# Optimization experiments

Hardware: AMD Instinct MI355X
Metric: run time of the kernel (lower is better)

## Reference

```python
import jax, jax.numpy as jnp
import numpy as np

HEAD_SIZE = 128
B, L = 4, 4096

def setup_inputs() -> dict:
    key = jax.random.key(0)
    k1, k2, k3 = jax.random.split(key, 3)
    return {
        "key": jax.random.normal(k1, (B, L, HEAD_SIZE), dtype=jnp.float32),
        "query": jax.random.normal(k2, (B, L, HEAD_SIZE), dtype=jnp.float32),
        "value": jax.random.normal(k3, (B, L, HEAD_SIZE), dtype=jnp.float32),
    }

def reference(key, query, value):
    # attention scores: [B, L, L]
    scale = 1.0 / jnp.sqrt(jnp.asarray(HEAD_SIZE, dtype=query.dtype))
    att = jnp.einsum("bqd,bkd->bqk", query, key) * scale
    # causal mask (tril): positions k > q get -inf
    causal = jnp.tril(jnp.ones((att.shape[1], att.shape[2]), dtype=bool))
    att = jnp.where(causal[None, :, :], att, jnp.array(-jnp.inf, dtype=att.dtype))
    logits = jax.nn.softmax(att, axis=-1)
    # dropout omitted (eval mode / deterministic reference)
    out = jnp.einsum("bqk,bkd->bqd", logits, value)
    return out
```

## Files before the change

kernel.cpp:

```cpp
#include <hip/hip_runtime.h>

#define BB 4
#define LL 4096
#define DD 128

typedef __attribute__((ext_vector_type(8))) short short8;
typedef __attribute__((ext_vector_type(4))) float f32x4;

typedef __attribute__((address_space(1))) const unsigned int gas_u32;
typedef __attribute__((address_space(3))) unsigned int las_u32;

__device__ __forceinline__ void gload_lds16(const void* g, void* l) {
  __builtin_amdgcn_global_load_lds((gas_u32*)g, (las_u32*)l, 16, 0, 0);
}

__device__ __forceinline__ unsigned short f2bf(float x) {
  union { float f; unsigned int u; } c; c.f = x;
  unsigned int r = (c.u + 0x7FFFu + ((c.u >> 16) & 1u)) >> 16;
  return (unsigned short)r;
}
__device__ __forceinline__ float bf2f(unsigned short h) {
  union { unsigned int u; float f; } c; c.u = (unsigned int)h << 16;
  return c.f;
}

__host__ __device__ __forceinline__ int slotBase(int p) {
  int g2 = (p - 4) >> 2, w2 = (p - 4) & 3;
  return 2 * g2 * g2 + 6 * g2 + w2 * (g2 + 2);
}

__global__ __launch_bounds__(256) void prep(const float* __restrict__ K,
                                            const float* __restrict__ V,
                                            unsigned short* __restrict__ Kb,
                                            unsigned short* __restrict__ Vt) {
  __shared__ unsigned short tile[64 * 130];
  int b  = blockIdx.x >> 6;
  int kt = (blockIdx.x & 63) << 6;
  int t = threadIdx.x;
  {
    int key = t >> 2, part = t & 3;
    const float* src = K + ((size_t)b * LL + kt + key) * DD + part * 32;
    unsigned short* dst = Kb + ((size_t)b * LL + kt + key) * DD + part * 32;
#pragma unroll
    for (int j = 0; j < 4; ++j) {
      float4 x = *(const float4*)(src + j * 8);
      float4 y = *(const float4*)(src + j * 8 + 4);
      union { unsigned short h[8]; uint4 v; } o;
      o.h[0] = f2bf(x.x); o.h[1] = f2bf(x.y); o.h[2] = f2bf(x.z); o.h[3] = f2bf(x.w);
      o.h[4] = f2bf(y.x); o.h[5] = f2bf(y.y); o.h[6] = f2bf(y.z); o.h[7] = f2bf(y.w);
      *(uint4*)(dst + j * 8) = o.v;
    }
  }
  int keyi = t >> 5, dim = (t & 31) * 4;
#pragma unroll
  for (int j = 0; j < 8; ++j) {
    int key = keyi + j * 8;
    float4 x = *(const float4*)(V + ((size_t)b * LL + kt + key) * DD + dim);
    uint2 pk;
    pk.x = f2bf(x.x) | ((unsigned int)f2bf(x.y) << 16);
    pk.y = f2bf(x.z) | ((unsigned int)f2bf(x.w) << 16);
    *(uint2*)(tile + key * 130 + dim) = pk;
  }
  __syncthreads();
  int kg = (t & 7) * 8, d0 = t >> 3;
#pragma unroll
  for (int j = 0; j < 4; ++j) {
    int d = d0 + j * 32;
    union { unsigned short h[8]; uint4 v; } o;
#pragma unroll
    for (int i = 0; i < 8; ++i) o.h[i] = tile[(kg + i) * 130 + d];
    *(uint4*)(Vt + ((size_t)b * DD + d) * LL + kt + kg) = o.v;
  }
}

__global__ __launch_bounds__(256, 3) void attn_fwd(const float* __restrict__ Q,
                                                   const unsigned short* __restrict__ Kb,
                                                   const unsigned short* __restrict__ Vt,
                                                   float* __restrict__ Out,
                                                   unsigned short* __restrict__ partO,
                                                   float* __restrict__ stats,
                                                   int split) {
  __shared__ unsigned short Ks[64 * 128];
  __shared__ unsigned short Vs[128 * 64];
  __shared__ unsigned short Ps[4][32 * 72];

  int tid = threadIdx.x;
  int wave = tid >> 6;
  int lane = tid & 63;
  int l = lane & 15, gq = lane >> 4;
  int lx = l & 7;

  int rem = (int)blockIdx.x, p = 31, nch;
  while (true) {
    nch = split ? ((2 * p + 2 + 7) >> 3) : 1;
    int n = 4 * nch;
    if (rem < n) break;
    rem -= n; --p;
  }
  int b = rem / nch, c = rem % nch;
  int T = 2 * p + 2;
  int nIters = split ? min(8, T - c * 8) : T;
  int ktBase = c << 9;
  int q0w = (p << 7) + wave * 32;
  int wkend = q0w + 31;
  int slot = (split && nch > 1) ? (b * 140 + slotBase(p) + c) : 0;

  const float SC = 0.08838834764831845f * 1.4426950408889634f;
  short8 qf[2][4];
#pragma unroll
  for (int mt = 0; mt < 2; ++mt) {
    const float* qp = Q + ((size_t)b * LL + q0w + mt * 16 + l) * DD + gq * 8;
#pragma unroll
    for (int cc = 0; cc < 4; ++cc) {
      float4 x = *(const float4*)(qp + cc * 32);
      float4 y = *(const float4*)(qp + cc * 32 + 4);
      short8 f;
      f[0] = (short)f2bf(x.x * SC); f[1] = (short)f2bf(x.y * SC);
      f[2] = (short)f2bf(x.z * SC); f[3] = (short)f2bf(x.w * SC);
      f[4] = (short)f2bf(y.x * SC); f[5] = (short)f2bf(y.y * SC);
      f[6] = (short)f2bf(y.z * SC); f[7] = (short)f2bf(y.w * SC);
      qf[mt][cc] = f;
    }
  }

  f32x4 acc[2][8];
#pragma unroll
  for (int mt = 0; mt < 2; ++mt)
#pragma unroll
    for (int i = 0; i < 8; ++i) acc[mt][i] = (f32x4){0.f, 0.f, 0.f, 0.f};
  f32x4 den[2];
  den[0] = (f32x4){0.f, 0.f, 0.f, 0.f};
  den[1] = (f32x4){0.f, 0.f, 0.f, 0.f};

  short8 ones;
#pragma unroll
  for (int j = 0; j < 8; ++j) ones[j] = (short)0x3F80;

  unsigned short* Pw = Ps[wave];
  const unsigned short* kgbase = Kb + (size_t)b * LL * DD;
  const unsigned short* vgbase = Vt + (size_t)b * DD * LL;

  for (int it = 0; it < nIters; ++it) {
    int kt = ktBase + it * 64;

    __syncthreads();
#pragma unroll
    for (int j = 0; j < 4; ++j) {
      int pk_ = j * 256 + tid;
      int krow = pk_ >> 4;
      int kcol = (pk_ & 15) ^ (krow & 7);
      gload_lds16(kgbase + (size_t)(kt + krow) * DD + kcol * 8, &Ks[pk_ * 8]);
      int vrow = pk_ >> 3;
      int vcol = (pk_ & 7) ^ (vrow & 7);
      gload_lds16(vgbase + (size_t)vrow * LL + kt + vcol * 8, &Vs[pk_ * 8]);
    }
    __syncthreads();

    if (kt > wkend) continue;

    bool diag = (kt + 63 > q0w);

#pragma unroll
    for (int nt = 0; nt < 4; ++nt) {
      const unsigned short* kp = Ks + (nt * 16 + l) * 128;
      f32x4 a0 = (f32x4){0.f, 0.f, 0.f, 0.f};
      f32x4 a1 = (f32x4){0.f, 0.f, 0.f, 0.f};
#pragma unroll
      for (int cc = 0; cc < 4; ++cc) {
        short8 kf = *(const short8*)(kp + (((gq + 4 * cc) ^ lx) << 3));
        a0 = __builtin_amdgcn_mfma_f32_16x16x32_bf16(qf[0][cc], kf, a0, 0, 0, 0);
        a1 = __builtin_amdgcn_mfma_f32_16x16x32_bf16(qf[1][cc], kf, a1, 0, 0, 0);
      }
      if (diag) {
        int key = kt + nt * 16 + l;
        int qr0 = q0w + gq * 4, qr1 = q0w + 16 + gq * 4;
#pragma unroll
        for (int r = 0; r < 4; ++r) {
          if (key > qr0 + r) a0[r] = -1e30f;
          if (key > qr1 + r) a1[r] = -1e30f;
        }
      }
#pragma unroll
      for (int r = 0; r < 4; ++r) {
        Pw[(gq * 4 + r) * 72 + nt * 16 + l] = f2bf(exp2f(a0[r]));
        Pw[(16 + gq * 4 + r) * 72 + nt * 16 + l] = f2bf(exp2f(a1[r]));
      }
    }

#pragma unroll
    for (int kc = 0; kc < 2; ++kc) {
      short8 pa0 = *(const short8*)(Pw + l * 72 + kc * 32 + gq * 8);
      short8 pa1 = *(const short8*)(Pw + (16 + l) * 72 + kc * 32 + gq * 8);
      den[0] = __builtin_amdgcn_mfma_f32_16x16x32_bf16(pa0, ones, den[0], 0, 0, 0);
      den[1] = __builtin_amdgcn_mfma_f32_16x16x32_bf16(pa1, ones, den[1], 0, 0, 0);
#pragma unroll
      for (int dt = 0; dt < 8; ++dt) {
        short8 vb = *(const short8*)(Vs + (dt * 16 + l) * 64 + (((kc * 4 + gq) ^ lx) << 3));
        acc[0][dt] = __builtin_amdgcn_mfma_f32_16x16x32_bf16(pa0, vb, acc[0][dt], 0, 0, 0);
        acc[1][dt] = __builtin_amdgcn_mfma_f32_16x16x32_bf16(pa1, vb, acc[1][dt], 0, 0, 0);
      }
    }
  }

  if (!split || nch == 1) {
    float* op = Out + ((size_t)b * LL + q0w) * DD;
#pragma unroll
    for (int mt = 0; mt < 2; ++mt) {
      float inv[4];
#pragma unroll
      for (int r = 0; r < 4; ++r) inv[r] = 1.0f / den[mt][r];
#pragma unroll
      for (int dt = 0; dt < 8; ++dt)
#pragma unroll
        for (int r = 0; r < 4; ++r)
          op[(size_t)(mt * 16 + gq * 4 + r) * DD + dt * 16 + l] = acc[mt][dt][r] * inv[r];
    }
  } else {
    unsigned short* pp = partO + (size_t)slot * 16384;
#pragma unroll
    for (int mt = 0; mt < 2; ++mt) {
      int rb = wave * 32 + mt * 16;
#pragma unroll
      for (int dt = 0; dt < 8; ++dt)
#pragma unroll
        for (int r = 0; r < 4; ++r)
          pp[(rb + gq * 4 + r) * 128 + dt * 16 + l] = f2bf(acc[mt][dt][r]);
      if (l == 0) {
#pragma unroll
        for (int r = 0; r < 4; ++r)
          stats[(size_t)slot * 128 + rb + gq * 4 + r] = den[mt][r];
      }
    }
  }
}

__global__ __launch_bounds__(256) void merge(const unsigned short* __restrict__ partO,
                                             const float* __restrict__ stats,
                                             float* __restrict__ Out) {
  int b = blockIdx.x / 112;
  int rest = blockIdx.x % 112;
  int p = 4 + rest / 4;
  int rg = rest % 4;
  int nch = (2 * p + 2 + 7) >> 3;
  int slot0 = b * 140 + slotBase(p);

  int tid = threadIdx.x;
  int row = rg * 32 + (tid >> 3);
  int dcol = (tid & 7) * 16;

  float lsum = 0.f;
  for (int cc = 0; cc < nch; ++cc)
    lsum += stats[(size_t)(slot0 + cc) * 128 + row];
  float inv = 1.0f / lsum;

  float o[16];
#pragma unroll
  for (int j = 0; j < 16; ++j) o[j] = 0.f;
  for (int cc = 0; cc < nch; ++cc) {
    const unsigned short* pp = partO + (size_t)(slot0 + cc) * 16384 + (size_t)row * 128 + dcol;
#pragma unroll
    for (int j = 0; j < 16; ++j) o[j] += bf2f(pp[j]);
  }
  float* op = Out + ((size_t)b * LL + (p << 7) + row) * DD + dcol;
#pragma unroll
  for (int j = 0; j < 4; ++j) {
    float4 v; v.x = o[j*4] * inv; v.y = o[j*4+1] * inv; v.z = o[j*4+2] * inv; v.w = o[j*4+3] * inv;
    *(float4*)(op + j * 4) = v;
  }
}

extern "C" void kernel_launch(void* const* d_in, const int* in_sizes, int n_in,
                              void* d_out, int out_size, void* d_ws, size_t ws_size,
                              hipStream_t stream) {
  const float* K = (const float*)d_in[0];
  const float* Q = (const float*)d_in[1];
  const float* V = (const float*)d_in[2];
  float* Out = (float*)d_out;

  const size_t convBytes = (size_t)2 * BB * LL * DD * 2;
  unsigned short* Kb = (unsigned short*)d_ws;
  unsigned short* Vt = Kb + (size_t)BB * LL * DD;

  size_t slots = (size_t)BB * 140;
  size_t need = convBytes + slots * 16384 * 2 + slots * 128 * 4;
  int split = (ws_size >= need) ? 1 : 0;

  unsigned short* partO = (unsigned short*)((char*)d_ws + convBytes);
  float* stats = (float*)((char*)d_ws + convBytes + slots * 16384 * 2);

  int nBlocks = 0;
  for (int p = 0; p < 32; ++p) nBlocks += 4 * (split ? ((2 * p + 2 + 7) >> 3) : 1);

  prep<<<dim3(BB * (LL / 64)), dim3(256), 0, stream>>>(K, V, Kb, Vt);
  attn_fwd<<<dim3(nBlocks), dim3(256), 0, stream>>>(Q, Kb, Vt, Out, partO, stats, split);
  if (split)
    merge<<<dim3(BB * 112), dim3(256), 0, stream>>>(partO, stats, Out);
}
```

Before: 121.8 us.

## Retile prep kernel, pack bf16 conversions, and store partials in MFMA fragment layout

```diff
diff --git a/kernel.cpp b/kernel.cpp
--- a/kernel.cpp
+++ b/kernel.cpp
@@ -1,4 +1,5 @@
 #include <hip/hip_runtime.h>
+#include <hip/hip_bf16.h>
 
 #define BB 4
 #define LL 4096
@@ -23,6 +24,12 @@
   union { unsigned int u; float f; } c; c.u = (unsigned int)h << 16;
   return c.f;
 }
+__device__ __forceinline__ unsigned int pk2bf(float a, float b) {
+  __hip_bfloat162 h = __float22bfloat162_rn(make_float2(a, b));
+  unsigned int u;
+  __builtin_memcpy(&u, &h, sizeof(u));
+  return u;
+}
 
 __host__ __device__ __forceinline__ int slotBase(int p) {
   int g2 = (p - 4) >> 2, w2 = (p - 4) & 3;
@@ -33,43 +40,50 @@
                                             const float* __restrict__ V,
                                             unsigned short* __restrict__ Kb,
                                             unsigned short* __restrict__ Vt) {
-  __shared__ unsigned short tile[64 * 130];
-  int b  = blockIdx.x >> 6;
-  int kt = (blockIdx.x & 63) << 6;
+  __shared__ unsigned short tile[32 * 132];
+  int b  = blockIdx.x >> 7;
+  int kt = (blockIdx.x & 127) << 5;
   int t = threadIdx.x;
+
   {
-    int key = t >> 2, part = t & 3;
-    const float* src = K + ((size_t)b * LL + kt + key) * DD + part * 32;
-    unsigned short* dst = Kb + ((size_t)b * LL + kt + key) * DD + part * 32;
+    size_t base = ((size_t)b * LL + kt) * DD + t * 16;
+    const float* src = K + base;
+    float4 x0 = *(const float4*)(src);
+    float4 x1 = *(const float4*)(src + 4);
+    float4 x2 = *(const float4*)(src + 8);
+    float4 x3 = *(const float4*)(src + 12);
+    union { unsigned short h[16]; uint4 v[2]; } o;
+    o.h[0]=f2bf(x0.x); o.h[1]=f2bf(x0.y); o.h[2]=f2bf(x0.z); o.h[3]=f2bf(x0.w);
+    o.h[4]=f2bf(x1.x); o.h[5]=f2bf(x1.y); o.h[6]=f2bf(x1.z); o.h[7]=f2bf(x1.w);
+    o.h[8]=f2bf(x2.x); o.h[9]=f2bf(x2.y); o.h[10]=f2bf(x2.z); o.h[11]=f2bf(x2.w);
+    o.h[12]=f2bf(x3.x); o.h[13]=f2bf(x3.y); o.h[14]=f2bf(x3.z); o.h[15]=f2bf(x3.w);
+    *(uint4*)(Kb + base) = o.v[0];
+    *(uint4*)(Kb + base + 8) = o.v[1];
+  }
+
+  {
+    int key = t >> 3, dim = (t & 7) * 16;
+    const float* src = V + ((size_t)b * LL + kt + key) * DD + dim;
 #pragma unroll
     for (int j = 0; j < 4; ++j) {
-      float4 x = *(const float4*)(src + j * 8);
-      float4 y = *(const float4*)(src + j * 8 + 4);
-      union { unsigned short h[8]; uint4 v; } o;
-      o.h[0] = f2bf(x.x); o.h[1] = f2bf(x.y); o.h[2] = f2bf(x.z); o.h[3] = f2bf(x.w);
-      o.h[4] = f2bf(y.x); o.h[5] = f2bf(y.y); o.h[6] = f2bf(y.z); o.h[7] = f2bf(y.w);
-      *(uint4*)(dst + j * 8) = o.v;
-    }
-  }
-  int keyi = t >> 5, dim = (t & 31) * 4;
-#pragma unroll
-  for (int j = 0; j < 8; ++j) {
-    int key = keyi + j * 8;
-    float4 x = *(const float4*)(V + ((size_t)b * LL + kt + key) * DD + dim);
-    uint2 pk;
-    pk.x = f2bf(x.x) | ((unsigned int)f2bf(x.y) << 16);
-    pk.y = f2bf(x.z) | ((unsigned int)f2bf(x.w) << 16);
-    *(uint2*)(tile + key * 130 + dim) = pk;
+      float4 x = *(const float4*)(src + j * 4);
+      uint2 pk;
+      pk.x = f2bf(x.x) | ((unsigned int)f2bf(x.y) << 16);
+      pk.y = f2bf(x.z) | ((unsigned int)f2bf(x.w) << 16);
+      *(uint2*)(tile + key * 132 + dim + j * 4) = pk;
+    }
   }
   __syncthreads();
-  int kg = (t & 7) * 8, d0 = t >> 3;
-#pragma unroll
-  for (int j = 0; j < 4; ++j) {
-    int d = d0 + j * 32;
-    union { unsigned short h[8]; uint4 v; } o;
-#pragma unroll
-    for (int i = 0; i < 8; ++i) o.h[i] = tile[(kg + i) * 130 + d];
-    *(uint4*)(Vt + ((size_t)b * DD + d) * LL + kt + kg) = o.v;
+  {
+    int d = t >> 1, h = t & 1;
+#pragma unroll
+    for (int j = 0; j < 2; ++j) {
+      int g = h * 2 + j;
+      union { unsigned short h2[8]; uint4 v; } o;
+#pragma unroll
+      for (int i = 0; i < 8; ++i) o.h2[i] = tile[(g * 8 + i) * 132 + d];
+      *(uint4*)(Vt + ((size_t)b * DD + d) * LL + kt + g * 8) = o.v;
+    }
   }
 }
 
@@ -91,7 +105,7 @@
   int lx = l & 7;
 
   int rem = (int)blockIdx.x, p = 31, nch;
-  while (true) {
+  for (;;) {
     nch = split ? ((2 * p + 2 + 7) >> 3) : 1;
     int n = 4 * nch;
     if (rem < n) break;
@@ -103,7 +117,8 @@
   int ktBase = c << 9;
   int q0w = (p << 7) + wave * 32;
   int wkend = q0w + 31;
-  int slot = (split && nch > 1) ? (b * 140 + slotBase(p) + c) : 0;
+  int multi = (split && nch > 1);
+  int slot = multi ? (b * 140 + slotBase(p) + c) : 0;
 
   const float SC = 0.08838834764831845f * 1.4426950408889634f;
   short8 qf[2][4];
@@ -182,8 +197,9 @@
       }
 #pragma unroll
       for (int r = 0; r < 4; ++r) {
-        Pw[(gq * 4 + r) * 72 + nt * 16 + l] = f2bf(exp2f(a0[r]));
-        Pw[(16 + gq * 4 + r) * 72 + nt * 16 + l] = f2bf(exp2f(a1[r]));
+        unsigned int pk = pk2bf(exp2f(a0[r]), exp2f(a1[r]));
+        Pw[(gq * 4 + r) * 72 + nt * 16 + l] = (unsigned short)pk;
+        Pw[(16 + gq * 4 + r) * 72 + nt * 16 + l] = (unsigned short)(pk >> 16);
       }
     }
 
@@ -202,7 +218,7 @@
     }
   }
 
-  if (!split || nch == 1) {
+  if (!multi) {
     float* op = Out + ((size_t)b * LL + q0w) * DD;
 #pragma unroll
     for (int mt = 0; mt < 2; ++mt) {
@@ -215,21 +231,23 @@
         for (int r = 0; r < 4; ++r)
           op[(size_t)(mt * 16 + gq * 4 + r) * DD + dt * 16 + l] = acc[mt][dt][r] * inv[r];
     }
-  } else {
-    unsigned short* pp = partO + (size_t)slot * 16384;
-#pragma unroll
-    for (int mt = 0; mt < 2; ++mt) {
-      int rb = wave * 32 + mt * 16;
-#pragma unroll
-      for (int dt = 0; dt < 8; ++dt)
-#pragma unroll
-        for (int r = 0; r < 4; ++r)
-          pp[(rb + gq * 4 + r) * 128 + dt * 16 + l] = f2bf(acc[mt][dt][r]);
-      if (l == 0) {
-#pragma unroll
-        for (int r = 0; r < 4; ++r)
-          stats[(size_t)slot * 128 + rb + gq * 4 + r] = den[mt][r];
-      }
+    return;
+  }
+
+  unsigned short* pp = partO + (size_t)slot * 16384;
+#pragma unroll
+  for (int mt = 0; mt < 2; ++mt) {
+#pragma unroll
+    for (int dt = 0; dt < 8; ++dt) {
+      uint2 v;
+      v.x = pk2bf(acc[mt][dt][0], acc[mt][dt][1]);
+      v.y = pk2bf(acc[mt][dt][2], acc[mt][dt][3]);
+      *(uint2*)(pp + ((((wave * 2 + mt) * 8 + dt) * 64 + lane) << 2)) = v;
+    }
+    if (l == 0) {
+#pragma unroll
+      for (int r = 0; r < 4; ++r)
+        stats[(size_t)slot * 128 + wave * 32 + mt * 16 + gq * 4 + r] = den[mt][r];
     }
   }
 }
@@ -239,33 +257,43 @@
                                              float* __restrict__ Out) {
   int b = blockIdx.x / 112;
   int rest = blockIdx.x % 112;
-  int p = 4 + rest / 4;
-  int rg = rest % 4;
+  int p = 4 + (rest >> 2);
+  int rg = rest & 2 ? (rest & 3) : (rest & 3);
+  rg = rest & 3;
   int nch = (2 * p + 2 + 7) >> 3;
   int slot0 = b * 140 + slotBase(p);
 
   int tid = threadIdx.x;
-  int row = rg * 32 + (tid >> 3);
-  int dcol = (tid & 7) * 16;
-
-  float lsum = 0.f;
-  for (int cc = 0; cc < nch; ++cc)
-    lsum += stats[(size_t)(slot0 + cc) * 128 + row];
-  float inv = 1.0f / lsum;
-
-  float o[16];
-#pragma unroll
-  for (int j = 0; j < 16; ++j) o[j] = 0.f;
-  for (int cc = 0; cc < nch; ++cc) {
-    const unsigned short* pp = partO + (size_t)(slot0 + cc) * 16384 + (size_t)row * 128 + dcol;
-#pragma unroll
-    for (int j = 0; j < 16; ++j) o[j] += bf2f(pp[j]);
-  }
-  float* op = Out + ((size_t)b * LL + (p << 7) + row) * DD + dcol;
+  int lane = tid & 63;
+  int l = lane & 15, gq = lane >> 4;
+  int w2 = tid >> 6;
+
 #pragma unroll
   for (int j = 0; j < 4; ++j) {
-    float4 v; v.x = o[j*4] * inv; v.y = o[j*4+1] * inv; v.z = o[j*4+2] * inv; v.w = o[j*4+3] * inv;
-    *(float4*)(op + j * 4) = v;
+    int pi = w2 * 4 + j;
+    int mt = pi >> 3, dt = pi & 7;
+
+    float den[4] = {0.f, 0.f, 0.f, 0.f};
+    for (int cc = 0; cc < nch; ++cc) {
+      const float* sp = stats + (size_t)(slot0 + cc) * 128 + rg * 32 + mt * 16 + gq * 4;
+#pragma unroll
+      for (int r = 0; r < 4; ++r) den[r] += sp[r];
+    }
+
+    float o[4] = {0.f, 0.f, 0.f, 0.f};
+    int off = (((rg * 2 + mt) * 8 + dt) * 64 + lane) << 2;
+    for (int cc = 0; cc < nch; ++cc) {
+      uint2 v = *(const uint2*)(partO + (size_t)(slot0 + cc) * 16384 + off);
+      o[0] += bf2f((unsigned short)v.x);
+      o[1] += bf2f((unsigned short)(v.x >> 16));
+      o[2] += bf2f((unsigned short)v.y);
+      o[3] += bf2f((unsigned short)(v.y >> 16));
+    }
+
+    float* op = Out + ((size_t)b * LL + (p << 7) + rg * 32 + mt * 16 + gq * 4) * DD + dt * 16 + l;
+#pragma unroll
+    for (int r = 0; r < 4; ++r)
+      op[(size_t)r * DD] = o[r] / den[r];
   }
 }
 
@@ -282,16 +310,16 @@
   unsigned short* Vt = Kb + (size_t)BB * LL * DD;
 
   size_t slots = (size_t)BB * 140;
-  size_t need = convBytes + slots * 16384 * 2 + slots * 128 * 4;
+  size_t need = convBytes + slots * 32768 + slots * 512;
   int split = (ws_size >= need) ? 1 : 0;
 
   unsigned short* partO = (unsigned short*)((char*)d_ws + convBytes);
-  float* stats = (float*)((char*)d_ws + convBytes + slots * 16384 * 2);
+  float* stats = (float*)((char*)d_ws + convBytes + slots * 32768);
 
   int nBlocks = 0;
   for (int p = 0; p < 32; ++p) nBlocks += 4 * (split ? ((2 * p + 2 + 7) >> 3) : 1);
 
-  prep<<<dim3(BB * (LL / 64)), dim3(256), 0, stream>>>(K, V, Kb, Vt);
+  prep<<<dim3(BB * (LL / 32)), dim3(256), 0, stream>>>(K, V, Kb, Vt);
   attn_fwd<<<dim3(nBlocks), dim3(256), 0, stream>>>(Q, Kb, Vt, Out, partO, stats, split);
   if (split)
     merge<<<dim3(BB * 112), dim3(256), 0, stream>>>(partO, stats, Out);
```

After: 134.1 us. +10.1%, slower.
